# Optimization experiments

Hardware: AMD Instinct MI355X
Metric: run time of the kernel (lower is better)

## Reference

```python
import jax, jax.numpy as jnp
import numpy as np

N_HEADS = 16
N_KV_HEADS = 4
HEAD_DIM = 128
ROPE_BASE = 10000.0


def _rms_norm(x):
    eps = jnp.asarray(jnp.finfo(x.dtype).eps, x.dtype)
    return x * jax.lax.rsqrt(jnp.mean(x * x, axis=-1, keepdims=True) + eps)


def _rope_tables(T, dtype):
    d = HEAD_DIM
    inv_freq = 1.0 / (ROPE_BASE ** (jnp.arange(0, d, 2, dtype=jnp.float32) / d))
    freqs = jnp.outer(jnp.arange(T, dtype=jnp.float32), inv_freq)  # [T, d/2]
    return jnp.cos(freqs).astype(dtype), jnp.sin(freqs).astype(dtype)


def _apply_rope(x, cos, sin):
    # x: [B, H, T, D]; cos/sin: [T, D/2]
    d = x.shape[-1] // 2
    x1, x2 = x[..., :d], x[..., d:]
    return jnp.concatenate((x1 * cos + x2 * sin, -x1 * sin + x2 * cos), axis=-1)


def setup_inputs() -> dict:
    key = jax.random.key(0)
    ks = jax.random.split(key, 5)
    B, T, C = 2, 2048, 2048
    kv_dim = N_KV_HEADS * HEAD_DIM
    s = 0.02
    return {
        "x": jax.random.normal(ks[0], (B, T, C), jnp.float32),
        "Wq": jax.random.normal(ks[1], (C, C), jnp.float32) * s,
        "Wk": jax.random.normal(ks[2], (kv_dim, C), jnp.float32) * s,
        "Wv": jax.random.normal(ks[3], (kv_dim, C), jnp.float32) * s,
        "Wo": jax.random.normal(ks[4], (C, C), jnp.float32) * s,
    }


def reference(x, Wq, Wk, Wv, Wo):
    B, T, C = x.shape
    g = N_HEADS // N_KV_HEADS

    # QKV projections (torch Linear: x @ W.T), split into heads -> [B, H, T, D]
    q = (x @ Wq.T).reshape(B, T, N_HEADS, HEAD_DIM).transpose(0, 2, 1, 3)
    k = (x @ Wk.T).reshape(B, T, N_KV_HEADS, HEAD_DIM).transpose(0, 2, 1, 3)
    v = (x @ Wv.T).reshape(B, T, N_KV_HEADS, HEAD_DIM).transpose(0, 2, 1, 3)

    # QK RMSNorm (no learned weight)
    q, k = _rms_norm(q), _rms_norm(k)

    # RoPE
    cos, sin = _rope_tables(T, q.dtype)
    q, k = _apply_rope(q, cos, sin), _apply_rope(k, cos, sin)

    # GQA: expand kv heads
    k = jnp.repeat(k, g, axis=1)
    v = jnp.repeat(v, g, axis=1)

    # causal SDPA
    scale = 1.0 / jnp.sqrt(jnp.asarray(HEAD_DIM, q.dtype))
    scores = jnp.einsum("bhqd,bhkd->bhqk", q, k) * scale
    mask = jnp.tril(jnp.ones((T, T), bool))
    scores = jnp.where(mask, scores, jnp.asarray(-jnp.inf, scores.dtype))
    att = jax.nn.softmax(scores, axis=-1)
    y = jnp.einsum("bhqk,bhkd->bhqd", att, v)

    y = y.transpose(0, 2, 1, 3).reshape(B, T, C)
    return y @ Wo.T
```

## Files before the change

### kernel.cpp

```cpp
#include <hip/hip_runtime.h>
#include <hip/hip_bf16.h>
#include <cstdint>
#include <math.h>

#define DEVINL __device__ __forceinline__

typedef __attribute__((ext_vector_type(8))) __bf16 bf16x8;
typedef __attribute__((ext_vector_type(4))) float floatx4;

constexpr int TB = 2;
constexpr int TT = 2048;
constexpr int TC = 2048;
constexpr int NH = 16, NKV = 4, HD = 128;
constexpr int MR = TB * TT;
constexpr int NQ = NH * HD;
constexpr int NK = NKV * HD;
constexpr int NQKV = NQ + 2 * NK;

DEVINL unsigned bfbits(float f) {
  unsigned u = __builtin_bit_cast(unsigned, f);
  return (u + 0x7FFFu + ((u >> 16) & 1u)) >> 16;
}
DEVINL int pk2(float a, float b) {
  union { __hip_bfloat162 h; int i; } u;
  u.h = __float22bfloat162_rn(float2{a, b});
  return u.i;
}
DEVINL void gl_lds16(const __hip_bfloat16* g, __hip_bfloat16* l) {
  __builtin_amdgcn_global_load_lds(
      (const __attribute__((address_space(1))) unsigned int*)g,
      (__attribute__((address_space(3))) unsigned int*)l, 16, 0, 0);
}
DEVINL floatx4 mfma16(bf16x8 a, bf16x8 b, floatx4 c) {
  return __builtin_amdgcn_mfma_f32_16x16x32_bf16(a, b, c, 0, 0, 0);
}
DEVINL void cstore(float* p, float v) { *p = v; }
DEVINL void cstore(__hip_bfloat16* p, float v) { *(unsigned short*)p = (unsigned short)bfbits(v); }

__global__ __launch_bounds__(256) void k_cvt5(
    const float* __restrict__ s0, const float* __restrict__ s1,
    const float* __restrict__ s2, const float* __restrict__ s3,
    const float* __restrict__ s4,
    __hip_bfloat16* __restrict__ d0, __hip_bfloat16* __restrict__ d1,
    __hip_bfloat16* __restrict__ d2, __hip_bfloat16* __restrict__ d3,
    __hip_bfloat16* __restrict__ d4) {
  const float* s;
  __hip_bfloat16* d;
  int n;
  switch (blockIdx.y) {
    case 0: s = s0; d = d0; n = MR * TC; break;
    case 1: s = s1; d = d1; n = NQ * TC; break;
    case 2: s = s2; d = d2; n = NK * TC; break;
    case 3: s = s3; d = d3; n = NK * TC; break;
    default: s = s4; d = d4; n = TC * TC; break;
  }
  int i = (blockIdx.x * 256 + threadIdx.x) * 4;
  if (i >= n) return;
  float4 v = *(const float4*)(s + i);
  ushort4 o;
  o.x = (unsigned short)bfbits(v.x);
  o.y = (unsigned short)bfbits(v.y);
  o.z = (unsigned short)bfbits(v.z);
  o.w = (unsigned short)bfbits(v.w);
  *(ushort4*)(d + i) = o;
}

template <typename OUT_T>
__global__ __launch_bounds__(256, 2) void k_gemm_bt(
    const __hip_bfloat16* __restrict__ A, const __hip_bfloat16* __restrict__ B,
    OUT_T* __restrict__ C, int M, int N, int K) {
  __shared__ __align__(16) __hip_bfloat16 As[128 * 32];
  __shared__ __align__(16) __hip_bfloat16 Bs[128 * 32];
  const int tid = threadIdx.x;
  const int lane = tid & 63, w = tid >> 6;
  const int q15 = lane & 15, quad = lane >> 4;
  const int wm = w >> 1, wn = w & 1;
  const int tm = blockIdx.y, tn = blockIdx.x;

  const int r0 = tid >> 2, c0 = (tid & 3) * 8;
  const __hip_bfloat16* a0 = A + (size_t)(tm * 128 + r0) * K + c0;
  const __hip_bfloat16* a1 = A + (size_t)(tm * 128 + r0 + 64) * K + c0;
  const __hip_bfloat16* b0 = B + (size_t)(tn * 128 + r0) * K + c0;
  const __hip_bfloat16* b1 = B + (size_t)(tn * 128 + r0 + 64) * K + c0;
  __hip_bfloat16* lA0 = As + (tid & ~63) * 8;
  __hip_bfloat16* lA1 = As + 2048 + (tid & ~63) * 8;
  __hip_bfloat16* lB0 = Bs + (tid & ~63) * 8;
  __hip_bfloat16* lB1 = Bs + 2048 + (tid & ~63) * 8;

  floatx4 acc[4][4] = {};
  for (int k0 = 0; k0 < K; k0 += 32) {
    __syncthreads();
    gl_lds16(a0 + k0, lA0);
    gl_lds16(a1 + k0, lA1);
    gl_lds16(b0 + k0, lB0);
    gl_lds16(b1 + k0, lB1);
    __syncthreads();
    bf16x8 af[4], bfr[4];
#pragma unroll
    for (int i = 0; i < 4; i++)
      af[i] = *(const bf16x8*)(As + (wm * 64 + i * 16 + q15) * 32 + quad * 8);
#pragma unroll
    for (int i = 0; i < 4; i++)
      bfr[i] = *(const bf16x8*)(Bs + (wn * 64 + i * 16 + q15) * 32 + quad * 8);
#pragma unroll
    for (int mi = 0; mi < 4; mi++)
#pragma unroll
      for (int ni = 0; ni < 4; ni++)
        acc[mi][ni] = mfma16(af[mi], bfr[ni], acc[mi][ni]);
  }
#pragma unroll
  for (int mi = 0; mi < 4; mi++) {
    int row0 = tm * 128 + wm * 64 + mi * 16 + quad * 4;
#pragma unroll
    for (int ni = 0; ni < 4; ni++) {
      int col = tn * 128 + wn * 64 + ni * 16 + q15;
#pragma unroll
      for (int r = 0; r < 4; r++)
        cstore(C + (size_t)(row0 + r) * N + col, acc[mi][ni][r]);
    }
  }
}

constexpr int ROPE_BLOCKS = (MR * 20) / 4;
__global__ __launch_bounds__(256) void k_prep(
    const __hip_bfloat16* __restrict__ qkv,
    __hip_bfloat16* __restrict__ q_l, __hip_bfloat16* __restrict__ k_l,
    __hip_bfloat16* __restrict__ vt) {
  if (blockIdx.x < ROPE_BLOCKS) {
    int gw = (blockIdx.x * 256 + threadIdx.x) >> 6;
    int lane = threadIdx.x & 63;
    int head = gw % 20;
    int bt = gw / 20;
    int b = bt >> 11, t = bt & (TT - 1);
    bool isq = head < NH;
    int h = isq ? head : head - NH;
    const __hip_bfloat16* src = qkv + (size_t)bt * NQKV + (isq ? h * HD : NQ + h * HD);
    float x1 = __bfloat162float(src[lane]);
    float x2 = __bfloat162float(src[lane + 64]);
    float ss = x1 * x1 + x2 * x2;
#pragma unroll
    for (int m = 1; m < 64; m <<= 1) ss += __shfl_xor(ss, m, 64);
    float rinv = rsqrtf(ss * (1.0f / 128.0f) + 1.1920928955078125e-07f);
    float ang = (float)t * exp2f((float)lane * -(13.287712379549449f / 64.0f));
    float sv = sinf(ang), cv = cosf(ang);
    float scale = isq ? (1.4426950408889634f * 0.08838834764831845f) : 1.0f;
    float o1 = (x1 * cv + x2 * sv) * rinv * scale;
    float o2 = (x2 * cv - x1 * sv) * rinv * scale;
    __hip_bfloat16* dst = isq ? q_l + ((size_t)(b * NH + h) * TT + t) * HD
                              : k_l + ((size_t)(b * NKV + h) * TT + t) * HD;
    *(unsigned short*)(dst + lane) = (unsigned short)bfbits(o1);
    *(unsigned short*)(dst + lane + 64) = (unsigned short)bfbits(o2);
  } else {
    __shared__ __hip_bfloat16 tile[64][130];
    int bid = blockIdx.x - ROPE_BLOCKS;
    int t0 = (bid & 31) * 64;
    int hk = (bid >> 5) & 3;
    int b = bid >> 7;
    int tid = threadIdx.x;
#pragma unroll
    for (int j = 0; j < 32; j++) {
      int e = j * 256 + tid;
      int tt = e >> 7, d = e & 127;
      tile[tt][d] = qkv[(size_t)(b * TT + t0 + tt) * NQKV + NQ + NK + hk * HD + d];
    }
    __syncthreads();
#pragma unroll
    for (int j = 0; j < 32; j++) {
      int e = j * 256 + tid;
      int d = e >> 6, tt = e & 63;
      vt[(((size_t)(b * NKV + hk)) * HD + d) * TT + t0 + tt] = tile[tt][d];
    }
  }
}

__global__ __launch_bounds__(256, 2) void k_attn(
    const __hip_bfloat16* __restrict__ q_l, const __hip_bfloat16* __restrict__ k_l,
    const __hip_bfloat16* __restrict__ vt_l, __hip_bfloat16* __restrict__ y) {
  __shared__ __align__(16) __hip_bfloat16 Ks[2][64 * 128];
  __shared__ __align__(16) __hip_bfloat16 Vs[2][128 * 64];
  const int tid = threadIdx.x, lane = tid & 63, w = tid >> 6;
  const int q15 = lane & 15, quad = lane >> 4;
  const int p = blockIdx.x;
  const int h = blockIdx.y, b = blockIdx.z;
  const int hk = h >> 2;

  const __hip_bfloat16* kbase = k_l + (size_t)(b * NKV + hk) * TT * HD;
  const __hip_bfloat16* vbase = vt_l + (size_t)(b * NKV + hk) * HD * TT;

  auto stage = [&](int kb, int buf) {
#pragma unroll
    for (int i = 0; i < 4; i++) {
      int s = i * 256 + tid;
      int rk = s >> 4, ck = s & 15;
      gl_lds16(kbase + (size_t)(kb * 64 + rk) * HD + (ck ^ (rk & 15)) * 8,
               Ks[buf] + (i * 256 + (tid & ~63)) * 8);
      int rv = s >> 3, cv = s & 7;
      gl_lds16(vbase + (size_t)rv * TT + kb * 64 + (cv ^ (rv & 7)) * 8,
               Vs[buf] + (i * 256 + (tid & ~63)) * 8);
    }
  };

  const int s0lane = ((quad & 1) << 1) * 16 + q15;
  const int s1lane = s0lane + 16;
  const bool hi = quad >= 2;
  int cur = 0;

  for (int ph = 0; ph < 2; ph++) {
    const int qb = ph ? (TT / 64 - 1 - p) : p;
    const __hip_bfloat16* qbase = q_l + ((size_t)(b * NH + h) * TT + qb * 64) * HD;

    bf16x8 qf[4];
#pragma unroll
    for (int dc = 0; dc < 4; dc++)
      qf[dc] = *(const bf16x8*)(qbase + (size_t)(w * 16 + q15) * HD + dc * 32 + quad * 8);

    floatx4 ot[8] = {};
    float lsum = 0.0f;

    for (int kb = 0; kb <= qb; kb++) {
      __syncthreads();
      if (kb == 0) {
        stage(0, cur);
        __syncthreads();
      }
      if (kb < qb) stage(kb + 1, cur ^ 1);

      floatx4 st[4] = {};
#pragma unroll
      for (int kt = 0; kt < 4; kt++) {
        int r = kt * 16 + q15;
#pragma unroll
        for (int dc = 0; dc < 4; dc++) {
          int c = dc * 4 + quad;
          bf16x8 kf = *(const bf16x8*)(Ks[cur] + (r * 16 + (c ^ (r & 15))) * 8);
          st[kt] = mfma16(kf, qf[dc], st[kt]);
        }
      }
      if (kb == qb) {
        int qg = w * 16 + q15;
#pragma unroll
        for (int kt = 0; kt < 4; kt++)
#pragma unroll
          for (int r = 0; r < 4; r++)
            if (kt * 16 + quad * 4 + r > qg) st[kt][r] = -INFINITY;
      }
      int pk[4][2];
#pragma unroll
      for (int kt = 0; kt < 4; kt++) {
        float p0 = exp2f(st[kt][0]);
        float p1 = exp2f(st[kt][1]);
        float p2 = exp2f(st[kt][2]);
        float p3 = exp2f(st[kt][3]);
        lsum += (p0 + p1) + (p2 + p3);
        pk[kt][0] = pk2(p0, p1);
        pk[kt][1] = pk2(p2, p3);
      }
#pragma unroll
      for (int kc = 0; kc < 2; kc++) {
        int lo0 = __shfl(pk[kc * 2][0], s0lane, 64);
        int lo1 = __shfl(pk[kc * 2][1], s0lane, 64);
        int lo2 = __shfl(pk[kc * 2][0], s1lane, 64);
        int lo3 = __shfl(pk[kc * 2][1], s1lane, 64);
        int h0 = __shfl(pk[kc * 2 + 1][0], s0lane, 64);
        int h1 = __shfl(pk[kc * 2 + 1][1], s0lane, 64);
        int h2 = __shfl(pk[kc * 2 + 1][0], s1lane, 64);
        int h3 = __shfl(pk[kc * 2 + 1][1], s1lane, 64);
        union { int i[4]; bf16x8 v; } pu;
        pu.i[0] = hi ? h0 : lo0;
        pu.i[1] = hi ? h1 : lo1;
        pu.i[2] = hi ? h2 : lo2;
        pu.i[3] = hi ? h3 : lo3;
        bf16x8 pf = pu.v;
#pragma unroll
        for (int dt = 0; dt < 8; dt++) {
          int r = dt * 16 + q15, c = kc * 4 + quad;
          bf16x8 vf = *(const bf16x8*)(Vs[cur] + (r * 8 + (c ^ (r & 7))) * 8);
          ot[dt] = mfma16(vf, pf, ot[dt]);
        }
      }
      cur ^= 1;
    }
    lsum += __shfl_xor(lsum, 16, 64);
    lsum += __shfl_xor(lsum, 32, 64);
    float linv = 1.0f / lsum;
    int t = qb * 64 + w * 16 + q15;
    __hip_bfloat16* yrow = y + (size_t)(b * TT + t) * TC + h * HD;
#pragma unroll
    for (int dt = 0; dt < 8; dt++) {
      int d = dt * 16 + quad * 4;
      ushort4 o;
      o.x = (unsigned short)bfbits(ot[dt][0] * linv);
      o.y = (unsigned short)bfbits(ot[dt][1] * linv);
      o.z = (unsigned short)bfbits(ot[dt][2] * linv);
      o.w = (unsigned short)bfbits(ot[dt][3] * linv);
      *(ushort4*)(yrow + d) = o;
    }
  }
}

extern "C" void kernel_launch(void* const* d_in, const int* in_sizes, int n_in,
                              void* d_out, int out_size, void* d_ws, size_t ws_size,
                              hipStream_t stream) {
  (void)in_sizes; (void)n_in; (void)out_size; (void)ws_size;
  const float* x  = (const float*)d_in[0];
  const float* Wq = (const float*)d_in[1];
  const float* Wk = (const float*)d_in[2];
  const float* Wv = (const float*)d_in[3];
  const float* Wo = (const float*)d_in[4];
  float* out = (float*)d_out;

  char* ws = (char*)d_ws;
  size_t off = 0;
  auto alloc = [&](size_t bytes) {
    void* p = ws + off;
    off += (bytes + 255) & ~(size_t)255;
    return p;
  };
  __hip_bfloat16* xb   = (__hip_bfloat16*)alloc((size_t)MR * TC * 2);
  __hip_bfloat16* wqkv = (__hip_bfloat16*)alloc((size_t)NQKV * TC * 2);
  __hip_bfloat16* wo   = (__hip_bfloat16*)alloc((size_t)TC * TC * 2);
  __hip_bfloat16* qkv  = (__hip_bfloat16*)alloc((size_t)MR * NQKV * 2);
  __hip_bfloat16* q_l  = (__hip_bfloat16*)alloc((size_t)TB * NH * TT * HD * 2);
  __hip_bfloat16* k_l  = (__hip_bfloat16*)alloc((size_t)TB * NKV * TT * HD * 2);
  __hip_bfloat16* vt_l = (__hip_bfloat16*)alloc((size_t)TB * NKV * HD * TT * 2);
  __hip_bfloat16* yb   = (__hip_bfloat16*)alloc((size_t)MR * TC * 2);

  k_cvt5<<<dim3((MR * TC / 4 + 255) / 256, 5), 256, 0, stream>>>(
      x, Wq, Wk, Wv, Wo,
      xb, wqkv, wqkv + (size_t)NQ * TC, wqkv + (size_t)(NQ + NK) * TC, wo);

  k_gemm_bt<__hip_bfloat16><<<dim3(NQKV / 128, MR / 128), 256, 0, stream>>>(
      xb, wqkv, qkv, MR, NQKV, TC);

  k_prep<<<ROPE_BLOCKS + TB * NKV * (TT / 64), 256, 0, stream>>>(qkv, q_l, k_l, vt_l);

  k_attn<<<dim3(TT / 64 / 2, NH, TB), 256, 0, stream>>>(q_l, k_l, vt_l, yb);

  k_gemm_bt<float><<<dim3(TC / 128, MR / 128), 256, 0, stream>>>(
      yb, wo, out, MR, TC, TC);
}
```

Baseline: 320.6 us.

## Enlarge attention query tile to 128 rows and route P through LDS

New measurement: 319.3 us. No clear change (-0.4%).

```diff
diff --git a/kernel.cpp b/kernel.cpp
--- a/kernel.cpp
+++ b/kernel.cpp
@@ -178,14 +178,18 @@
     const __hip_bfloat16* __restrict__ vt_l, __hip_bfloat16* __restrict__ y) {
   __shared__ __align__(16) __hip_bfloat16 Ks[2][64 * 128];
   __shared__ __align__(16) __hip_bfloat16 Vs[2][128 * 64];
+  __shared__ __align__(16) __hip_bfloat16 Ps[4][32 * 64];
   const int tid = threadIdx.x, lane = tid & 63, w = tid >> 6;
   const int q15 = lane & 15, quad = lane >> 4;
-  const int p = blockIdx.x;
-  const int h = blockIdx.y, b = blockIdx.z;
+  const int id = blockIdx.x;
+  const int qt = (TT / 128 - 1) - (id >> 5);
+  const int h = id & 15, b = (id >> 4) & 1;
   const int hk = h >> 2;
+  const int nkb = 2 * qt + 2;
 
   const __hip_bfloat16* kbase = k_l + (size_t)(b * NKV + hk) * TT * HD;
   const __hip_bfloat16* vbase = vt_l + (size_t)(b * NKV + hk) * HD * TT;
+  const __hip_bfloat16* qbase = q_l + ((size_t)(b * NH + h) * TT + qt * 128) * HD;
 
   auto stage = [&](int kb, int buf) {
 #pragma unroll
@@ -200,32 +204,34 @@
     }
   };
 
-  const int s0lane = ((quad & 1) << 1) * 16 + q15;
-  const int s1lane = s0lane + 16;
-  const bool hi = quad >= 2;
+  bf16x8 qf[4][2];
+#pragma unroll
+  for (int dc = 0; dc < 4; dc++)
+#pragma unroll
+    for (int qh = 0; qh < 2; qh++)
+      qf[dc][qh] = *(const bf16x8*)(qbase + (size_t)(w * 32 + qh * 16 + q15) * HD +
+                                    dc * 32 + quad * 8);
+
+  __hip_bfloat16* pw = Ps[w];
+  const int qrow0 = q15, qrow1 = 16 + q15;
+  const int pw_c = 2 * 0 + (quad >> 1);
+  const int pw_h = (quad & 1) * 4;
+
+  floatx4 ot[8][2] = {};
+  float lsum[2] = {0.0f, 0.0f};
   int cur = 0;
-
-  for (int ph = 0; ph < 2; ph++) {
-    const int qb = ph ? (TT / 64 - 1 - p) : p;
-    const __hip_bfloat16* qbase = q_l + ((size_t)(b * NH + h) * TT + qb * 64) * HD;
-
-    bf16x8 qf[4];
-#pragma unroll
-    for (int dc = 0; dc < 4; dc++)
-      qf[dc] = *(const bf16x8*)(qbase + (size_t)(w * 16 + q15) * HD + dc * 32 + quad * 8);
-
-    floatx4 ot[8] = {};
-    float lsum = 0.0f;
-
-    for (int kb = 0; kb <= qb; kb++) {
+  const int kb_last_w = 2 * qt + (w >> 1);
+
+  for (int kb = 0; kb < nkb; kb++) {
+    __syncthreads();
+    if (kb == 0) {
+      stage(0, cur);
       __syncthreads();
-      if (kb == 0) {
-        stage(0, cur);
-        __syncthreads();
-      }
-      if (kb < qb) stage(kb + 1, cur ^ 1);
-
-      floatx4 st[4] = {};
+    }
+    if (kb + 1 < nkb) stage(kb + 1, cur ^ 1);
+
+    if (kb <= kb_last_w) {
+      floatx4 st[4][2] = {};
 #pragma unroll
       for (int kt = 0; kt < 4; kt++) {
         int r = kt * 16 + q15;
@@ -233,66 +239,74 @@
         for (int dc = 0; dc < 4; dc++) {
           int c = dc * 4 + quad;
           bf16x8 kf = *(const bf16x8*)(Ks[cur] + (r * 16 + (c ^ (r & 15))) * 8);
-          st[kt] = mfma16(kf, qf[dc], st[kt]);
+          st[kt][0] = mfma16(kf, qf[dc][0], st[kt][0]);
+          st[kt][1] = mfma16(kf, qf[dc][1], st[kt][1]);
         }
       }
-      if (kb == qb) {
-        int qg = w * 16 + q15;
-#pragma unroll
-        for (int kt = 0; kt < 4; kt++)
-#pragma unroll
-          for (int r = 0; r < 4; r++)
-            if (kt * 16 + quad * 4 + r > qg) st[kt][r] = -INFINITY;
+      if (kb >= 2 * qt) {
+#pragma unroll
+        for (int qh = 0; qh < 2; qh++) {
+          int qg = qt * 128 + w * 32 + qh * 16 + q15;
+#pragma unroll
+          for (int kt = 0; kt < 4; kt++)
+#pragma unroll
+            for (int r = 0; r < 4; r++)
+              if (kb * 64 + kt * 16 + quad * 4 + r > qg) st[kt][qh][r] = -INFINITY;
+        }
       }
-      int pk[4][2];
 #pragma unroll
       for (int kt = 0; kt < 4; kt++) {
-        float p0 = exp2f(st[kt][0]);
-        float p1 = exp2f(st[kt][1]);
-        float p2 = exp2f(st[kt][2]);
-        float p3 = exp2f(st[kt][3]);
-        lsum += (p0 + p1) + (p2 + p3);
-        pk[kt][0] = pk2(p0, p1);
-        pk[kt][1] = pk2(p2, p3);
+#pragma unroll
+        for (int qh = 0; qh < 2; qh++) {
+          float p0 = exp2f(st[kt][qh][0]);
+          float p1 = exp2f(st[kt][qh][1]);
+          float p2 = exp2f(st[kt][qh][2]);
+          float p3 = exp2f(st[kt][qh][3]);
+          lsum[qh] += (p0 + p1) + (p2 + p3);
+          int2 pv;
+          pv.x = pk2(p0, p1);
+          pv.y = pk2(p2, p3);
+          int row = qh * 16 + q15;
+          int c4 = (kt * 2 + (quad >> 1)) ^ (row & 7);
+          *(int2*)(pw + row * 64 + c4 * 8 + pw_h) = pv;
+        }
       }
 #pragma unroll
       for (int kc = 0; kc < 2; kc++) {
-        int lo0 = __shfl(pk[kc * 2][0], s0lane, 64);
-        int lo1 = __shfl(pk[kc * 2][1], s0lane, 64);
-        int lo2 = __shfl(pk[kc * 2][0], s1lane, 64);
-        int lo3 = __shfl(pk[kc * 2][1], s1lane, 64);
-        int h0 = __shfl(pk[kc * 2 + 1][0], s0lane, 64);
-        int h1 = __shfl(pk[kc * 2 + 1][1], s0lane, 64);
-        int h2 = __shfl(pk[kc * 2 + 1][0], s1lane, 64);
-        int h3 = __shfl(pk[kc * 2 + 1][1], s1lane, 64);
-        union { int i[4]; bf16x8 v; } pu;
-        pu.i[0] = hi ? h0 : lo0;
-        pu.i[1] = hi ? h1 : lo1;
-        pu.i[2] = hi ? h2 : lo2;
-        pu.i[3] = hi ? h3 : lo3;
-        bf16x8 pf = pu.v;
+        bf16x8 pf[2];
+#pragma unroll
+        for (int qh = 0; qh < 2; qh++) {
+          int row = qh * 16 + q15;
+          int c4 = (kc * 4 + quad) ^ (row & 7);
+          pf[qh] = *(const bf16x8*)(pw + row * 64 + c4 * 8);
+        }
 #pragma unroll
         for (int dt = 0; dt < 8; dt++) {
           int r = dt * 16 + q15, c = kc * 4 + quad;
           bf16x8 vf = *(const bf16x8*)(Vs[cur] + (r * 8 + (c ^ (r & 7))) * 8);
-          ot[dt] = mfma16(vf, pf, ot[dt]);
+          ot[dt][0] = mfma16(vf, pf[0], ot[dt][0]);
+          ot[dt][1] = mfma16(vf, pf[1], ot[dt][1]);
         }
       }
-      cur ^= 1;
-    }
-    lsum += __shfl_xor(lsum, 16, 64);
-    lsum += __shfl_xor(lsum, 32, 64);
-    float linv = 1.0f / lsum;
-    int t = qb * 64 + w * 16 + q15;
+    }
+    cur ^= 1;
+  }
+#pragma unroll
+  for (int qh = 0; qh < 2; qh++) {
+    float ls = lsum[qh];
+    ls += __shfl_xor(ls, 16, 64);
+    ls += __shfl_xor(ls, 32, 64);
+    float linv = 1.0f / ls;
+    int t = qt * 128 + w * 32 + qh * 16 + q15;
     __hip_bfloat16* yrow = y + (size_t)(b * TT + t) * TC + h * HD;
 #pragma unroll
     for (int dt = 0; dt < 8; dt++) {
       int d = dt * 16 + quad * 4;
       ushort4 o;
-      o.x = (unsigned short)bfbits(ot[dt][0] * linv);
-      o.y = (unsigned short)bfbits(ot[dt][1] * linv);
-      o.z = (unsigned short)bfbits(ot[dt][2] * linv);
-      o.w = (unsigned short)bfbits(ot[dt][3] * linv);
+      o.x = (unsigned short)bfbits(ot[dt][qh][0] * linv);
+      o.y = (unsigned short)bfbits(ot[dt][qh][1] * linv);
+      o.z = (unsigned short)bfbits(ot[dt][qh][2] * linv);
+      o.w = (unsigned short)bfbits(ot[dt][qh][3] * linv);
       *(ushort4*)(yrow + d) = o;
     }
   }
@@ -334,7 +348,7 @@
 
   k_prep<<<ROPE_BLOCKS + TB * NKV * (TT / 64), 256, 0, stream>>>(qkv, q_l, k_l, vt_l);
 
-  k_attn<<<dim3(TT / 64 / 2, NH, TB), 256, 0, stream>>>(q_l, k_l, vt_l, yb);
+  k_attn<<<(TT / 128) * NH * TB, 256, 0, stream>>>(q_l, k_l, vt_l, yb);
 
   k_gemm_bt<float><<<dim3(TC / 128, MR / 128), 256, 0, stream>>>(
       yb, wo, out, MR, TC, TC);
```
